# Kernel optimization log

Measured on AMD Instinct MI355X. Metric: run time of the kernel, lower is better.

The kernel has to match this reference:

```python
import jax, jax.numpy as jnp
import numpy as np

B, N, D_MODEL, D_INNER = 8, 1024, 512, 2048
N_HEAD, D_K, D_V = 8, 64, 64
N_EXPERTS, TOP_K = 24, 2
N_GROUPS = 4
EPS = 1e-6


def setup_inputs() -> dict:
    key = jax.random.key(0)
    ks = jax.random.split(key, 12)
    s = 0.02
    rn = lambda k, shp: jax.random.normal(k, shp, dtype=jnp.float32) * s
    inp = {
        "x": jax.random.normal(ks[0], (B, N, D_MODEL), dtype=jnp.float32),
        "wq": rn(ks[1], (D_MODEL, N_HEAD * D_K)),
        "wk": rn(ks[2], (D_MODEL, N_HEAD * D_K)),
        "wv": rn(ks[3], (D_MODEL, N_HEAD * D_V)),
        "wo": rn(ks[4], (N_HEAD * D_V, D_MODEL)),
        "ln_attn_g": jnp.ones((D_MODEL,), jnp.float32),
        "ln_attn_b": jnp.zeros((D_MODEL,), jnp.float32),
        "wg1": rn(ks[5], (D_MODEL, N_EXPERTS)),
        "w1": rn(ks[6], (N_EXPERTS, D_MODEL, D_INNER)),
        "b1": jnp.zeros((N_EXPERTS, D_INNER), jnp.float32),
        "wg2": rn(ks[7], (D_INNER, N_EXPERTS)),
        "w2": rn(ks[8], (N_EXPERTS, D_INNER, D_MODEL)),
        "b2": jnp.zeros((N_EXPERTS, D_MODEL), jnp.float32),
        "ln_out_g": jnp.ones((D_MODEL,), jnp.float32),
        "ln_out_b": jnp.zeros((D_MODEL,), jnp.float32),
    }
    for i in range(1, 5):
        inp[f"ln{i}_g"] = jnp.ones((D_INNER,), jnp.float32)
        inp[f"ln{i}_b"] = jnp.zeros((D_INNER,), jnp.float32)
    return inp


def _ln(x, g, b):
    m = jnp.mean(x, -1, keepdims=True)
    v = jnp.mean((x - m) ** 2, -1, keepdims=True)
    return (x - m) * jax.lax.rsqrt(v + EPS) * g + b


def _gate(xf, wg, capacity):
    # top-2 gating with capacity-limited one-hot dispatch (GShard-style)
    gates = jax.nn.softmax(xf @ wg)                      # [T,E]
    w, idx = jax.lax.top_k(gates, TOP_K)                 # [T,2]
    w = w / jnp.sum(w, -1, keepdims=True)
    m1 = jax.nn.one_hot(idx[:, 0], N_EXPERTS, dtype=xf.dtype)
    m2 = jax.nn.one_hot(idx[:, 1], N_EXPERTS, dtype=xf.dtype)
    loc1 = jnp.cumsum(m1, 0) - 1.0                       # slot within expert
    loc2 = jnp.cumsum(m2, 0) - 1.0 + jnp.sum(m1, 0)[None, :]
    m1 = m1 * (loc1 < capacity)
    m2 = m2 * (loc2 < capacity)
    c1 = w[:, 0, None, None] * m1[:, :, None] * jax.nn.one_hot(loc1.astype(jnp.int32), capacity, dtype=xf.dtype)
    c2 = w[:, 1, None, None] * m2[:, :, None] * jax.nn.one_hot(loc2.astype(jnp.int32), capacity, dtype=xf.dtype)
    combine = c1 + c2                                    # [T,E,C]
    dispatch = (combine > 0).astype(xf.dtype)
    return combine, dispatch


def _moe(xf, combine, dispatch, W, b):
    ein = jnp.einsum('tec,td->ecd', dispatch, xf)        # gather into expert slots
    out = jnp.einsum('ecd,edh->ech', ein, W) + b[:, None, :]
    return jnp.einsum('tec,ech->th', combine, out)       # weighted combine


def reference(x, wq, wk, wv, wo, ln_attn_g, ln_attn_b, wg1, w1, b1, wg2, w2, b2,
              ln1_g, ln1_b, ln2_g, ln2_b, ln3_g, ln3_b, ln4_g, ln4_b,
              ln_out_g, ln_out_b):
    # ---- multi-head self-attention ----
    temp = D_K ** 0.5
    q = (x @ wq).reshape(B, N, N_HEAD, D_K)
    k = (x @ wk).reshape(B, N, N_HEAD, D_K)
    v = (x @ wv).reshape(B, N, N_HEAD, D_V)
    attn = jax.nn.softmax(jnp.einsum('bnhd,bmhd->bhnm', q / temp, k), axis=-1)
    ctx = jnp.einsum('bhnm,bmhd->bnhd', attn, v).reshape(B, N, N_HEAD * D_V)
    ctx = jax.nn.relu(ctx @ wo) + x                      # dropout is identity at eval
    ctx = _ln(ctx, ln_attn_g, ln_attn_b)
    # ---- TaskMoE positionwise FFN over 4 sequence groups ----
    resid = ctx
    xg = ctx.reshape(B, N_GROUPS, N // N_GROUPS, D_MODEL)
    T = B * (N // N_GROUPS)
    cap = int(np.ceil(T * TOP_K / N_EXPERTS))
    ln_gs = [ln1_g, ln2_g, ln3_g, ln4_g]
    ln_bs = [ln1_b, ln2_b, ln3_b, ln4_b]
    outs = []
    for i in range(N_GROUPS):
        xf = xg[:, i].reshape(T, D_MODEL)
        combine, dispatch = _gate(xf, wg1, cap)          # routing reused by 2nd MoE
        h = _moe(xf, combine, dispatch, w1, b1)          # [T, D_INNER]
        h = jax.nn.relu(_ln(h, ln_gs[i], ln_bs[i]))
        o = _moe(h, combine, dispatch, w2, b2)           # [T, D_MODEL]
        outs.append(o.reshape(B, N // N_GROUPS, D_MODEL))
    y = jnp.concatenate(outs, axis=1) + resid
    return _ln(y, ln_out_g, ln_out_b)
```

## Files before the change

### kernel.cpp

```cpp
#include <hip/hip_runtime.h>
#include <cstdint>


#define NTOK 8192
#define DM   512
#define DI   2048
#define NEXP 24
#define TPG  2048
#define CAP  171
#define CAPR 176
#define EPSF 1e-6f

typedef __bf16 bf16x8 __attribute__((ext_vector_type(8)));
typedef float f32x4 __attribute__((ext_vector_type(4)));

static __device__ __forceinline__ unsigned short f2bf(float f) {
  unsigned int u = __builtin_bit_cast(unsigned int, f);
  u = (u + 0x7fffu + ((u >> 16) & 1u)) >> 16;
  return (unsigned short)u;
}
static __device__ __forceinline__ float bf2f(unsigned short u) {
  return __builtin_bit_cast(float, (unsigned int)u << 16);
}
static __device__ __forceinline__ unsigned int pk2(float a, float b) {
  return (unsigned int)f2bf(a) | ((unsigned int)f2bf(b) << 16);
}

static __device__ __forceinline__ void gload16(const unsigned short* g, unsigned short* l) {
  __builtin_amdgcn_global_load_lds(
      (const __attribute__((address_space(1))) void*)g,
      (__attribute__((address_space(3))) void*)l, 16, 0, 0);
}

__global__ __launch_bounds__(256) void convw(
    const float* __restrict__ in, unsigned short* __restrict__ out, int K, int N)
{
  __shared__ unsigned short T[64][65];
  int e = blockIdx.z;
  const float* ip = in + (size_t)e * K * N;
  unsigned short* op = out + (size_t)e * N * K;
  int n0 = blockIdx.x * 64, k0 = blockIdx.y * 64;
  int tid = threadIdx.x;
  #pragma unroll
  for (int i = 0; i < 16; ++i) {
    int lin = tid + i * 256;
    int k = lin >> 6, n = lin & 63;
    T[n][k] = f2bf(ip[(size_t)(k0 + k) * N + n0 + n]);
  }
  __syncthreads();
  #pragma unroll
  for (int i = 0; i < 16; ++i) {
    int lin = tid + i * 256;
    int n = lin >> 6, k = lin & 63;
    op[(size_t)(n0 + n) * K + k0 + k] = T[n][k];
  }
}

__global__ __launch_bounds__(256) void convx(
    const float* __restrict__ in, unsigned short* __restrict__ out)
{
  int i = blockIdx.x * 256 + threadIdx.x;
  float4 v = ((const float4*)in)[i];
  uint2 p;
  p.x = pk2(v.x, v.y); p.y = pk2(v.z, v.w);
  ((uint2*)out)[i] = p;
}

__global__ __launch_bounds__(256) void mfma_gemm(
    const unsigned short* __restrict__ A, int lda,
    const unsigned short* __restrict__ Bt,
    const float* __restrict__ bias,
    const int* __restrict__ lrow, const int* __restrict__ cnts,
    float* __restrict__ Cf, unsigned short* __restrict__ Cb,
    const float* __restrict__ Add,
    int M, int N, int K, int mode, float scale,
    int nx, int ny, int npair)
{
  __shared__ unsigned short As[64 * 64];
  __shared__ unsigned short Bs[128 * 64];
  int tid = threadIdx.x;
  int w = tid >> 6, lane = tid & 63, quad = lane >> 4, l16 = lane & 15;

  int bid = blockIdx.x;
  int xcd = bid & 7, s = bid >> 3;
  int n0, m0, pair;
  if (npair > 1) {
    int nxy = nx * ny;
    int pidx = s / nxy;
    int inner = s - pidx * nxy;
    pair = xcd + (pidx << 3);
    n0 = (inner % nx) * 128;
    m0 = (inner / nx) * 64;
  } else {
    int midx = s / nx;
    int inner = s - midx * nx;
    m0 = (xcd + (midx << 3)) * 64;
    n0 = inner * 128;
    pair = 0;
  }
  int e = pair % NEXP;
  int count = cnts ? cnts[pair] : M;
  if (m0 >= count) return;
  const int* lr = lrow ? lrow + pair * CAPR : nullptr;

  int sub = lane >> 3;
  int gsw = (lane & 7) ^ sub;
  const unsigned short* aSrc[2];
  #pragma unroll
  for (int i = 0; i < 2; ++i) {
    int mm = m0 + i * 32 + w * 8 + sub;
    if (mm >= count) mm = count - 1;
    int rm = lr ? lr[mm] : mm;
    aSrc[i] = A + (size_t)rm * lda + gsw * 8;
  }
  const unsigned short* Bte = Bt + (size_t)e * N * K;
  const unsigned short* bSrc[4];
  #pragma unroll
  for (int i = 0; i < 4; ++i)
    bSrc[i] = Bte + (size_t)(n0 + i * 32 + w * 8 + sub) * K + gsw * 8;

  int wbase = w * 512;

  f32x4 acc[4][2] = {};
  for (int t = 0; t < K; t += 64) {
    if (t) __syncthreads();
    #pragma unroll
    for (int i = 0; i < 2; ++i) gload16(aSrc[i] + t, &As[i * 2048 + wbase]);
    #pragma unroll
    for (int i = 0; i < 4; ++i) gload16(bSrc[i] + t, &Bs[i * 2048 + wbase]);
    asm volatile("s_waitcnt vmcnt(0)" ::: "memory");
    __syncthreads();
    #pragma unroll
    for (int half = 0; half < 2; ++half) {
      int g8 = ((half * 4 + quad) ^ (l16 & 7)) * 8;
      bf16x8 af[4];
      #pragma unroll
      for (int ms = 0; ms < 4; ++ms)
        af[ms] = *(const bf16x8*)&As[(ms * 16 + l16) * 64 + g8];
      bf16x8 bfr[2];
      #pragma unroll
      for (int ns = 0; ns < 2; ++ns)
        bfr[ns] = *(const bf16x8*)&Bs[(w * 32 + ns * 16 + l16) * 64 + g8];
      #pragma unroll
      for (int ms = 0; ms < 4; ++ms)
        #pragma unroll
        for (int ns = 0; ns < 2; ++ns)
          acc[ms][ns] = __builtin_amdgcn_mfma_f32_16x16x32_bf16(af[ms], bfr[ns], acc[ms][ns], 0, 0, 0);
    }
  }
  float bv[2] = {0.f, 0.f};
  unsigned short* Cbp = Cb;
  if (mode == 3) {
    #pragma unroll
    for (int ns = 0; ns < 2; ++ns)
      bv[ns] = bias[(size_t)e * N + n0 + w * 32 + ns * 16 + l16];
    Cbp = Cb + (size_t)pair * CAPR * N;
  }
  #pragma unroll
  for (int ms = 0; ms < 4; ++ms) {
    #pragma unroll
    for (int ns = 0; ns < 2; ++ns) {
      int col = n0 + w * 32 + ns * 16 + l16;
      #pragma unroll
      for (int r = 0; r < 4; ++r) {
        int m = m0 + ms * 16 + quad * 4 + r;
        if (mode == 0) {
          float sc = col < 512 ? scale : 1.0f;
          Cbp[(size_t)m * N + col] = f2bf(acc[ms][ns][r] * sc);
        } else if (mode == 1) {
          Cf[(size_t)m * N + col] = fmaxf(acc[ms][ns][r], 0.f) + Add[(size_t)m * N + col];
        } else {
          if (m < CAPR)
            Cbp[(size_t)m * N + col] = f2bf(acc[ms][ns][r] + bv[ns]);
        }
      }
    }
  }
}

__global__ __launch_bounds__(256) void attn_mfma(
    const unsigned short* __restrict__ QKV, unsigned short* __restrict__ ctx)
{
  __shared__ unsigned short Ks[64 * 72];
  __shared__ unsigned short Vt[64 * 72];
  __shared__ unsigned short Ps[4][16 * 72];
  int tid = threadIdx.x;
  int w = tid >> 6, lane = tid & 63, quad = lane >> 4, l16 = lane & 15;
  int bid = blockIdx.x;
  int xcd = bid & 7, s = bid >> 3;
  int bh = xcd + ((s >> 4) << 3);
  int qt = s & 15;
  int b = bh >> 3, h = bh & 7;
  size_t hoff = (size_t)h * 64;
  size_t tokbase = (size_t)b * 1024;

  int qrow = qt * 64 + w * 16 + l16;
  const unsigned short* qp = QKV + (tokbase + qrow) * 1536 + hoff + quad * 8;
  bf16x8 qa0 = *(const bf16x8*)(qp);
  bf16x8 qa1 = *(const bf16x8*)(qp + 32);

  f32x4 O[4] = {};
  float mrow[4], lrowv[4];
  #pragma unroll
  for (int r = 0; r < 4; ++r) { mrow[r] = -1e30f; lrowv[r] = 0.f; }

  for (int kv0 = 0; kv0 < 1024; kv0 += 64) {
    __syncthreads();
    {
      const unsigned short* kg = QKV + (tokbase + kv0) * 1536 + 512 + hoff;
      #pragma unroll
      for (int i = 0; i < 2; ++i) {
        int f = tid + i * 256;
        int key = f >> 3, c = f & 7;
        *(uint4*)&Ks[key * 72 + c * 8] = *(const uint4*)(kg + (size_t)key * 1536 + c * 8);
      }
      const unsigned short* vg = QKV + (tokbase + kv0) * 1536 + 1024 + hoff;
      int d = tid & 63;
      #pragma unroll
      for (int i = 0; i < 2; ++i) {
        int ko = (tid >> 6) + i * 4;
        const unsigned short* vq = vg + (size_t)ko * 8 * 1536 + d;
        unsigned int a0 = vq[0],         a1 = vq[1536];
        unsigned int a2 = vq[2 * 1536],  a3 = vq[3 * 1536];
        unsigned int a4 = vq[4 * 1536],  a5 = vq[5 * 1536];
        unsigned int a6 = vq[6 * 1536],  a7 = vq[7 * 1536];
        uint4 pk;
        pk.x = a0 | (a1 << 16); pk.y = a2 | (a3 << 16);
        pk.z = a4 | (a5 << 16); pk.w = a6 | (a7 << 16);
        *(uint4*)&Vt[d * 72 + ko * 8] = pk;
      }
    }
    __syncthreads();

    f32x4 s4[4];
    #pragma unroll
    for (int kt = 0; kt < 4; ++kt) {
      const unsigned short* kr = &Ks[(kt * 16 + l16) * 72 + quad * 8];
      bf16x8 kb0 = *(const bf16x8*)(kr);
      bf16x8 kb1 = *(const bf16x8*)(kr + 32);
      f32x4 z = {};
      z = __builtin_amdgcn_mfma_f32_16x16x32_bf16(qa0, kb0, z, 0, 0, 0);
      z = __builtin_amdgcn_mfma_f32_16x16x32_bf16(qa1, kb1, z, 0, 0, 0);
      s4[kt] = z;
    }

    #pragma unroll
    for (int r = 0; r < 4; ++r) {
      float mx = fmaxf(fmaxf(s4[0][r], s4[1][r]), fmaxf(s4[2][r], s4[3][r]));
      mx = fmaxf(mx, __shfl_xor(mx, 1, 64));
      mx = fmaxf(mx, __shfl_xor(mx, 2, 64));
      mx = fmaxf(mx, __shfl_xor(mx, 4, 64));
      mx = fmaxf(mx, __shfl_xor(mx, 8, 64));
      float mnew = fmaxf(mrow[r], mx);
      float alpha = __expf(mrow[r] - mnew);
      mrow[r] = mnew;
      float psum = 0.f;
      #pragma unroll
      for (int kt = 0; kt < 4; ++kt) {
        float p = __expf(s4[kt][r] - mnew);
        s4[kt][r] = p;
        psum += p;
      }
      psum += __shfl_xor(psum, 1, 64);
      psum += __shfl_xor(psum, 2, 64);
      psum += __shfl_xor(psum, 4, 64);
      psum += __shfl_xor(psum, 8, 64);
      lrowv[r] = lrowv[r] * alpha + psum;
      #pragma unroll
      for (int dt = 0; dt < 4; ++dt) O[dt][r] *= alpha;
    }

    #pragma unroll
    for (int kt = 0; kt < 4; ++kt)
      #pragma unroll
      for (int r = 0; r < 4; ++r)
        Ps[w][(quad * 4 + r) * 72 + kt * 16 + l16] = f2bf(s4[kt][r]);
    const unsigned short* pp = &Ps[w][l16 * 72 + quad * 8];
    bf16x8 pa0 = *(const bf16x8*)(pp);
    bf16x8 pa1 = *(const bf16x8*)(pp + 32);

    #pragma unroll
    for (int dt = 0; dt < 4; ++dt) {
      const unsigned short* vr = &Vt[(dt * 16 + l16) * 72 + quad * 8];
      bf16x8 vb0 = *(const bf16x8*)(vr);
      bf16x8 vb1 = *(const bf16x8*)(vr + 32);
      O[dt] = __builtin_amdgcn_mfma_f32_16x16x32_bf16(pa0, vb0, O[dt], 0, 0, 0);
      O[dt] = __builtin_amdgcn_mfma_f32_16x16x32_bf16(pa1, vb1, O[dt], 0, 0, 0);
    }
  }

  #pragma unroll
  for (int r = 0; r < 4; ++r) {
    float inv = 1.0f / lrowv[r];
    int row = qt * 64 + w * 16 + quad * 4 + r;
    unsigned short* cp = ctx + (tokbase + row) * 512 + hoff + l16;
    #pragma unroll
    for (int dt = 0; dt < 4; ++dt) cp[dt * 16] = f2bf(O[dt][r] * inv);
  }
}

__global__ __launch_bounds__(256) void ln_kernel(
    const float* __restrict__ in,
    float* __restrict__ out, unsigned short* __restrict__ outb,
    int D, const float* __restrict__ g, const float* __restrict__ bb)
{
  int row = blockIdx.x;
  const float* ip = in + (size_t)row * D;
  float vals[8];
  int per = D >> 8;
  float s1 = 0.f, s2 = 0.f;
  for (int i = 0; i < per; ++i) {
    int d = threadIdx.x + (i << 8);
    float vv = ip[d];
    vals[i] = vv; s1 += vv; s2 += vv * vv;
  }
  #pragma unroll
  for (int o = 32; o; o >>= 1) { s1 += __shfl_xor(s1, o, 64); s2 += __shfl_xor(s2, o, 64); }
  __shared__ float sA[4], sB[4];
  int wid = threadIdx.x >> 6, lane = threadIdx.x & 63;
  if (lane == 0) { sA[wid] = s1; sB[wid] = s2; }
  __syncthreads();
  float t1 = sA[0] + sA[1] + sA[2] + sA[3];
  float t2 = sB[0] + sB[1] + sB[2] + sB[3];
  float mean = t1 / (float)D;
  float var = t2 / (float)D - mean * mean;
  float rs = rsqrtf(var + EPSF);
  float* op = out ? out + (size_t)row * D : nullptr;
  unsigned short* obp = outb ? outb + (size_t)row * D : nullptr;
  for (int i = 0; i < per; ++i) {
    int d = threadIdx.x + (i << 8);
    float o = (vals[i] - mean) * rs * g[d] + bb[d];
    if (op)  op[d] = o;
    if (obp) obp[d] = f2bf(o);
  }
}

template<int PER>
__global__ __launch_bounds__(256) void combine_ln(
    const unsigned short* __restrict__ slots,
    const int* __restrict__ ts0, const int* __restrict__ ts1,
    const float* __restrict__ sw,
    const float* __restrict__ addf,
    float* __restrict__ outf, unsigned short* __restrict__ outb,
    int relu_after,
    const float* __restrict__ g0, const float* __restrict__ g1,
    const float* __restrict__ g2, const float* __restrict__ g3,
    const float* __restrict__ bb0, const float* __restrict__ bb1,
    const float* __restrict__ bb2, const float* __restrict__ bb3)
{
  const int D = PER * 256;
  int row = blockIdx.x;
  int grp = (row & 1023) >> 8;
  const float* g  = grp == 0 ? g0  : grp == 1 ? g1  : grp == 2 ? g2  : g3;
  const float* bb = grp == 0 ? bb0 : grp == 1 ? bb1 : grp == 2 ? bb2 : bb3;
  int s0 = ts0[row], s1 = ts1[row];
  float w0 = s0 >= 0 ? sw[s0] : 0.f;
  float w1 = s1 >= 0 ? sw[s1] : 0.f;
  const unsigned short* p0 = slots + (size_t)(s0 >= 0 ? s0 : 0) * D;
  const unsigned short* p1 = slots + (size_t)(s1 >= 0 ? s1 : 0) * D;
  int base = threadIdx.x * PER;

  float addv[PER];
  if (addf) {
    const float* ap = addf + (size_t)row * D + base;
    if constexpr (PER == 8) {
      float4 t0 = *(const float4*)(ap);
      float4 t1 = *(const float4*)(ap + 4);
      addv[0]=t0.x; addv[1]=t0.y; addv[2]=t0.z; addv[3]=t0.w;
      addv[4]=t1.x; addv[5]=t1.y; addv[6]=t1.z; addv[7]=t1.w;
    } else {
      float2 t0 = *(const float2*)(ap);
      addv[0]=t0.x; addv[1]=t0.y;
    }
  } else {
    #pragma unroll
    for (int i = 0; i < PER; ++i) addv[i] = 0.f;
  }
  unsigned short b0[PER] = {}, b1[PER] = {};
  if (s0 >= 0) {
    if constexpr (PER == 8) *(uint4*)b0 = *(const uint4*)(p0 + base);
    else *(unsigned int*)b0 = *(const unsigned int*)(p0 + base);
  }
  if (s1 >= 0) {
    if constexpr (PER == 8) *(uint4*)b1 = *(const uint4*)(p1 + base);
    else *(unsigned int*)b1 = *(const unsigned int*)(p1 + base);
  }

  float vals[PER];
  float sm1 = 0.f, sm2 = 0.f;
  #pragma unroll
  for (int i = 0; i < PER; ++i) {
    float v = addv[i];
    if (s0 >= 0) v += w0 * bf2f(b0[i]);
    if (s1 >= 0) v += w1 * bf2f(b1[i]);
    vals[i] = v; sm1 += v; sm2 += v * v;
  }
  #pragma unroll
  for (int o = 32; o; o >>= 1) { sm1 += __shfl_xor(sm1, o, 64); sm2 += __shfl_xor(sm2, o, 64); }
  __shared__ float sA[4], sB[4];
  int wid = threadIdx.x >> 6, lane = threadIdx.x & 63;
  if (lane == 0) { sA[wid] = sm1; sB[wid] = sm2; }
  __syncthreads();
  float t1 = sA[0] + sA[1] + sA[2] + sA[3];
  float t2 = sB[0] + sB[1] + sB[2] + sB[3];
  float mean = t1 / (float)D;
  float var = t2 / (float)D - mean * mean;
  float rs = rsqrtf(var + EPSF);

  float ov[PER];
  #pragma unroll
  for (int i = 0; i < PER; ++i) {
    float o = (vals[i] - mean) * rs * g[base + i] + bb[base + i];
    if (relu_after) o = fmaxf(o, 0.f);
    ov[i] = o;
  }
  if (outf) {
    float* op = outf + (size_t)row * D + base;
    if constexpr (PER == 8) {
      *(float4*)(op)     = make_float4(ov[0], ov[1], ov[2], ov[3]);
      *(float4*)(op + 4) = make_float4(ov[4], ov[5], ov[6], ov[7]);
    } else {
      *(float2*)(op) = make_float2(ov[0], ov[1]);
    }
  }
  if (outb) {
    unsigned short* obp = outb + (size_t)row * D + base;
    if constexpr (PER == 8) {
      uint4 o;
      o.x = pk2(ov[0], ov[1]); o.y = pk2(ov[2], ov[3]);
      o.z = pk2(ov[4], ov[5]); o.w = pk2(ov[6], ov[7]);
      *(uint4*)obp = o;
    } else {
      *(unsigned int*)obp = pk2(ov[0], ov[1]);
    }
  }
}

__global__ __launch_bounds__(256) void gate1(
    const float* __restrict__ xln, const float* __restrict__ wg,
    int* __restrict__ idx0, int* __restrict__ idx1,
    float* __restrict__ w0o, float* __restrict__ w1o)
{
  int wid = threadIdx.x >> 6, lane = threadIdx.x & 63;
  int tk = blockIdx.x * 4 + wid;
  int g = tk >> 11, t = tk & 2047;
  int b = t >> 8, j = t & 255;
  size_t row = (size_t)b * 1024 + g * 256 + j;
  const float* xp = xln + row * 512;
  float acc = -1e30f;
  if (lane < 24) {
    acc = 0.f;
    for (int d = 0; d < 512; ++d) acc += xp[d] * wg[d * 24 + lane];
  }
  float b0v = -1e30f, b1v = -1e30f; int i0 = 0, i1 = 0;
  for (int e = 0; e < 24; ++e) {
    float vv = __shfl(acc, e, 64);
    if (vv > b0v)      { b1v = b0v; i1 = i0; b0v = vv; i0 = e; }
    else if (vv > b1v) { b1v = vv; i1 = e; }
  }
  if (lane == 0) {
    float w0 = 1.0f / (1.0f + __expf(b1v - b0v));
    idx0[tk] = i0; idx1[tk] = i1; w0o[tk] = w0; w1o[tk] = 1.0f - w0;
  }
}

__global__ __launch_bounds__(64) void gate2(
    const int* __restrict__ idx0, const int* __restrict__ idx1,
    const float* __restrict__ w0, const float* __restrict__ w1,
    int* __restrict__ lrow, float* __restrict__ lw, int* __restrict__ counts,
    int* __restrict__ ts0, int* __restrict__ ts1)
{
  int pair = blockIdx.x; int g = pair / 24; int e = pair % 24;
  int lane = threadIdx.x;
  int base = g * TPG;
  unsigned long long lm = (lane == 63) ? 0x7fffffffffffffffULL : ((1ULL << lane) - 1ULL);
  int run = 0;
  for (int it = 0; it < TPG / 64; ++it) {
    int t = it * 64 + lane;
    bool m = (idx0[base + t] == e);
    unsigned long long mask = __ballot(m);
    int pre = __popcll(mask & lm);
    int rank = run + pre;
    if (m && rank < CAP) {
      int bq = t >> 8, j = t & 255;
      int rowidx = bq * 1024 + g * 256 + j;
      lrow[pair * CAPR + rank] = rowidx;
      lw[pair * CAPR + rank] = w0[base + t];
      ts0[rowidx] = pair * CAPR + rank;
    }
    run += __popcll(mask);
  }
  int total1 = run;
  int run2 = 0;
  for (int it = 0; it < TPG / 64; ++it) {
    int t = it * 64 + lane;
    bool m = (idx1[base + t] == e);
    unsigned long long mask = __ballot(m);
    int pre = __popcll(mask & lm);
    int rank2 = run2 + pre;
    if (m && (total1 + rank2) < CAP) {
      int bq = t >> 8, j = t & 255;
      int rowidx = bq * 1024 + g * 256 + j;
      lrow[pair * CAPR + total1 + rank2] = rowidx;
      lw[pair * CAPR + total1 + rank2] = w1[base + t];
      ts1[rowidx] = pair * CAPR + total1 + rank2;
    }
    run2 += __popcll(mask);
  }
  if (lane == 0) {
    int c1 = total1 < CAP ? total1 : CAP;
    int room = CAP - total1; if (room < 0) room = 0;
    int c2 = run2 < room ? run2 : room;
    counts[pair] = c1 + c2;
  }
}

extern "C" void kernel_launch(void* const* d_in, const int* in_sizes, int n_in,
                              void* d_out, int out_size, void* d_ws, size_t ws_size,
                              hipStream_t stream)
{
  const float* x   = (const float*)d_in[0];
  const float* wq  = (const float*)d_in[1];
  const float* wk  = (const float*)d_in[2];
  const float* wv  = (const float*)d_in[3];
  const float* wo  = (const float*)d_in[4];
  const float* ln_attn_g = (const float*)d_in[5];
  const float* ln_attn_b = (const float*)d_in[6];
  const float* wg1 = (const float*)d_in[7];
  const float* w1  = (const float*)d_in[8];
  const float* b1  = (const float*)d_in[9];
  const float* w2  = (const float*)d_in[11];
  const float* b2  = (const float*)d_in[12];
  const float* ln_out_g = (const float*)d_in[13];
  const float* ln_out_b = (const float*)d_in[14];
  const float* ln1g = (const float*)d_in[15]; const float* ln1b = (const float*)d_in[16];
  const float* ln2g = (const float*)d_in[17]; const float* ln2b = (const float*)d_in[18];
  const float* ln3g = (const float*)d_in[19]; const float* ln3b = (const float*)d_in[20];
  const float* ln4g = (const float*)d_in[21]; const float* ln4b = (const float*)d_in[22];

  char* ws = (char*)d_ws;
  const size_t MB = 1048576;
  unsigned short* wt1    = (unsigned short*)(ws + 0);
  unsigned short* hb2    = (unsigned short*)(ws + 0);
  unsigned short* wt2    = (unsigned short*)(ws + 48 * MB);
  float*          ctxln  = (float*)(ws + 96 * MB);
  unsigned short* ctxlnb = (unsigned short*)(ws + 112 * MB);
  unsigned short* xbf    = (unsigned short*)(ws + 120 * MB);
  unsigned short* out1   = (unsigned short*)(ws + 120 * MB);
  unsigned short* out2   = (unsigned short*)(ws + 120 * MB);
  unsigned short* qkvb   = (unsigned short*)(ws + 128 * MB);
  unsigned short* ctxb   = (unsigned short*)(ws + 152 * MB);
  unsigned short* wtqkv  = (unsigned short*)(ws + 160 * MB);
  unsigned short* wto    = (unsigned short*)(ws + 160 * MB + 1572864);
  float*          y0     = (float*)(ws + 162 * MB);
  char*  small = ws + 190 * MB;
  int*   idx0  = (int*)(small + 0);
  int*   idx1  = (int*)(small + 32768);
  float* w0a   = (float*)(small + 65536);
  float* w1a   = (float*)(small + 98304);
  int*   lrowp = (int*)(small + 131072);
  float* lwv   = (float*)(small + 198656);
  int*   cnts  = (int*)(small + 266240);
  int*   ts0   = (int*)(small + 270336);
  int*   ts1   = (int*)(small + 303104);

  dim3 blk(256);
  convw<<<dim3(8, 8, 1), blk, 0, stream>>>(wq, wtqkv, 512, 512);
  convw<<<dim3(8, 8, 1), blk, 0, stream>>>(wk, wtqkv + (size_t)512 * 512, 512, 512);
  convw<<<dim3(8, 8, 1), blk, 0, stream>>>(wv, wtqkv + (size_t)1024 * 512, 512, 512);
  convw<<<dim3(8, 8, 1), blk, 0, stream>>>(wo, wto, 512, 512);
  convw<<<dim3(32, 8, 24), blk, 0, stream>>>(w1, wt1, 512, 2048);
  convw<<<dim3(8, 32, 24), blk, 0, stream>>>(w2, wt2, 2048, 512);
  convx<<<4096, blk, 0, stream>>>(x, xbf);
  mfma_gemm<<<1536, blk, 0, stream>>>(xbf, DM, wtqkv, nullptr, nullptr, nullptr,
      nullptr, qkvb, nullptr, NTOK, 1536, DM, 0, 0.125f, 12, 128, 1);
  attn_mfma<<<1024, blk, 0, stream>>>(qkvb, ctxb);
  mfma_gemm<<<512, blk, 0, stream>>>(ctxb, DM, wto, nullptr, nullptr, nullptr,
      y0, nullptr, x, NTOK, DM, DM, 1, 1.0f, 4, 128, 1);
  ln_kernel<<<8192, blk, 0, stream>>>(y0, ctxln, ctxlnb, DM, ln_attn_g, ln_attn_b);
  gate1<<<2048, blk, 0, stream>>>(ctxln, wg1, idx0, idx1, w0a, w1a);
  hipMemsetAsync(ts0, 0xFF, 65536, stream);
  gate2<<<96, 64, 0, stream>>>(idx0, idx1, w0a, w1a, lrowp, lwv, cnts, ts0, ts1);
  mfma_gemm<<<4608, blk, 0, stream>>>(ctxlnb, DM, wt1, b1, lrowp, cnts,
      nullptr, out1, nullptr, 0, DI, DM, 3, 1.0f, 16, 3, 96);
  combine_ln<8><<<8192, blk, 0, stream>>>(out1, ts0, ts1, lwv, nullptr,
      nullptr, hb2, 1, ln1g, ln2g, ln3g, ln4g, ln1b, ln2b, ln3b, ln4b);
  mfma_gemm<<<1152, blk, 0, stream>>>(hb2, DI, wt2, b2, lrowp, cnts,
      nullptr, out2, nullptr, 0, DM, DI, 3, 1.0f, 4, 3, 96);
  combine_ln<2><<<8192, blk, 0, stream>>>(out2, ts0, ts1, lwv, ctxln,
      (float*)d_out, nullptr, 0, ln_out_g, ln_out_g, ln_out_g, ln_out_g,
      ln_out_b, ln_out_b, ln_out_b, ln_out_b);
}
```

Measured before the change: 686.9 us.

## Split attention KV range in two and merge partials in a combine kernel

The attention kernel now splits each query tile's key range into two halves processed by separate blocks. Each block writes unnormalized fp32 partial outputs plus its running max and sum, and a new combine kernel merges the two halves with log-sum-exp rescaling. K tiles are also read straight from global memory into MFMA operands instead of being staged through LDS, and launch bounds now request higher occupancy. This doubles the block count to improve occupancy and parallelism, at the cost of extra fp32 partial traffic and an additional kernel launch.

Measured after the change: 717.9 us. +4.5%, slower.

```diff
diff --git a/kernel.cpp b/kernel.cpp
--- a/kernel.cpp
+++ b/kernel.cpp
@@ -178,43 +178,42 @@
   }
 }
 
-__global__ __launch_bounds__(256) void attn_mfma(
-    const unsigned short* __restrict__ QKV, unsigned short* __restrict__ ctx)
-{
-  __shared__ unsigned short Ks[64 * 72];
+__global__ __launch_bounds__(256, 8) void attn_part(
+    const unsigned short* __restrict__ QKV,
+    float* __restrict__ Op0, float* __restrict__ Op1,
+    float* __restrict__ ml)
+{
   __shared__ unsigned short Vt[64 * 72];
   __shared__ unsigned short Ps[4][16 * 72];
   int tid = threadIdx.x;
   int w = tid >> 6, lane = tid & 63, quad = lane >> 4, l16 = lane & 15;
   int bid = blockIdx.x;
   int xcd = bid & 7, s = bid >> 3;
-  int bh = xcd + ((s >> 4) << 3);
-  int qt = s & 15;
+  int bh = xcd + ((s >> 5) << 3);
+  int inner = s & 31;
+  int split = inner >> 4;
+  int qt = inner & 15;
   int b = bh >> 3, h = bh & 7;
   size_t hoff = (size_t)h * 64;
   size_t tokbase = (size_t)b * 1024;
+  int kvbase = split << 9;
 
   int qrow = qt * 64 + w * 16 + l16;
   const unsigned short* qp = QKV + (tokbase + qrow) * 1536 + hoff + quad * 8;
   bf16x8 qa0 = *(const bf16x8*)(qp);
   bf16x8 qa1 = *(const bf16x8*)(qp + 32);
 
+  const unsigned short* kbase = QKV + (tokbase + kvbase + l16) * 1536 + 512 + hoff + quad * 8;
+
   f32x4 O[4] = {};
   float mrow[4], lrowv[4];
   #pragma unroll
   for (int r = 0; r < 4; ++r) { mrow[r] = -1e30f; lrowv[r] = 0.f; }
 
-  for (int kv0 = 0; kv0 < 1024; kv0 += 64) {
+  for (int kv0 = 0; kv0 < 512; kv0 += 64) {
     __syncthreads();
     {
-      const unsigned short* kg = QKV + (tokbase + kv0) * 1536 + 512 + hoff;
-      #pragma unroll
-      for (int i = 0; i < 2; ++i) {
-        int f = tid + i * 256;
-        int key = f >> 3, c = f & 7;
-        *(uint4*)&Ks[key * 72 + c * 8] = *(const uint4*)(kg + (size_t)key * 1536 + c * 8);
-      }
-      const unsigned short* vg = QKV + (tokbase + kv0) * 1536 + 1024 + hoff;
+      const unsigned short* vg = QKV + (tokbase + kvbase + kv0) * 1536 + 1024 + hoff;
       int d = tid & 63;
       #pragma unroll
       for (int i = 0; i < 2; ++i) {
@@ -235,7 +234,7 @@
     f32x4 s4[4];
     #pragma unroll
     for (int kt = 0; kt < 4; ++kt) {
-      const unsigned short* kr = &Ks[(kt * 16 + l16) * 72 + quad * 8];
+      const unsigned short* kr = kbase + (size_t)(kv0 + kt * 16) * 1536;
       bf16x8 kb0 = *(const bf16x8*)(kr);
       bf16x8 kb1 = *(const bf16x8*)(kr + 32);
       f32x4 z = {};
@@ -289,14 +288,39 @@
     }
   }
 
+  float* Opx = split ? Op1 : Op0;
+  float* mlb = ml + (size_t)(split * 2) * 65536;
   #pragma unroll
   for (int r = 0; r < 4; ++r) {
-    float inv = 1.0f / lrowv[r];
     int row = qt * 64 + w * 16 + quad * 4 + r;
-    unsigned short* cp = ctx + (tokbase + row) * 512 + hoff + l16;
-    #pragma unroll
-    for (int dt = 0; dt < 4; ++dt) cp[dt * 16] = f2bf(O[dt][r] * inv);
-  }
+    float* cp = Opx + (((size_t)bh << 10) + row) * 64 + l16;
+    #pragma unroll
+    for (int dt = 0; dt < 4; ++dt) cp[dt * 16] = O[dt][r];
+    if (l16 == 0) {
+      int idx = (bh << 10) | row;
+      mlb[idx] = mrow[r];
+      mlb[65536 + idx] = lrowv[r];
+    }
+  }
+}
+
+__global__ __launch_bounds__(256) void attn_comb(
+    const float* __restrict__ Op0, const float* __restrict__ Op1,
+    const float* __restrict__ ml, unsigned short* __restrict__ ctx)
+{
+  int idx = blockIdx.x * 4 + (threadIdx.x >> 6);
+  int lane = threadIdx.x & 63;
+  int bh = idx >> 10, row = idx & 1023;
+  int b = bh >> 3, h = bh & 7;
+  float m0 = ml[idx],          l0 = ml[65536 + idx];
+  float m1 = ml[131072 + idx], l1 = ml[196608 + idx];
+  float m = fmaxf(m0, m1);
+  float e0 = __expf(m0 - m), e1 = __expf(m1 - m);
+  float linv = 1.0f / (l0 * e0 + l1 * e1);
+  float o0 = Op0[(size_t)idx * 64 + lane];
+  float o1 = Op1[(size_t)idx * 64 + lane];
+  float v = (o0 * e0 + o1 * e1) * linv;
+  ctx[(((size_t)b << 10) + row) * 512 + h * 64 + lane] = f2bf(v);
 }
 
 __global__ __launch_bounds__(256) void ln_kernel(
@@ -544,6 +568,7 @@
   unsigned short* hb2    = (unsigned short*)(ws + 0);
   unsigned short* wt2    = (unsigned short*)(ws + 48 * MB);
   float*          ctxln  = (float*)(ws + 96 * MB);
+  float*          Op0    = (float*)(ws + 96 * MB);
   unsigned short* ctxlnb = (unsigned short*)(ws + 112 * MB);
   unsigned short* xbf    = (unsigned short*)(ws + 120 * MB);
   unsigned short* out1   = (unsigned short*)(ws + 120 * MB);
@@ -553,6 +578,8 @@
   unsigned short* wtqkv  = (unsigned short*)(ws + 160 * MB);
   unsigned short* wto    = (unsigned short*)(ws + 160 * MB + 1572864);
   float*          y0     = (float*)(ws + 162 * MB);
+  float*          Op1    = (float*)(ws + 162 * MB);
+  float*          mlbuf  = (float*)(ws + 180 * MB);
   char*  small = ws + 190 * MB;
   int*   idx0  = (int*)(small + 0);
   int*   idx1  = (int*)(small + 32768);
@@ -574,7 +601,8 @@
   convx<<<4096, blk, 0, stream>>>(x, xbf);
   mfma_gemm<<<1536, blk, 0, stream>>>(xbf, DM, wtqkv, nullptr, nullptr, nullptr,
       nullptr, qkvb, nullptr, NTOK, 1536, DM, 0, 0.125f, 12, 128, 1);
-  attn_mfma<<<1024, blk, 0, stream>>>(qkvb, ctxb);
+  attn_part<<<2048, blk, 0, stream>>>(qkvb, Op0, Op1, mlbuf);
+  attn_comb<<<16384, blk, 0, stream>>>(Op0, Op1, mlbuf, ctxb);
   mfma_gemm<<<512, blk, 0, stream>>>(ctxb, DM, wto, nullptr, nullptr, nullptr,
       y0, nullptr, x, NTOK, DM, DM, 1, 1.0f, 4, 128, 1);
   ln_kernel<<<8192, blk, 0, stream>>>(y0, ctxln, ctxlnb, DM, ln_attn_g, ln_attn_b);
```
